# Performance work log

Hardware: AMD Instinct MI355X
Metric: run time of the kernel (lower is better)

The kernel has to match this reference:

```python
import jax, jax.numpy as jnp
import numpy as np

T_STEPS = 16384  # sequence length T
N_DIM = 256      # input channels n
M_DIM = 512      # hidden/reservoir size m
K_MEM = 511      # memory rows K (addresses are 0..K, row 0 = 'no memory op')
L_OUT = 256      # output dims L


def setup_inputs() -> dict:
    key = jax.random.key(0)
    ks = jax.random.split(key, 10)
    s_ih = 1.0 / np.sqrt(N_DIM)
    s_hh = 1.0 / np.sqrt(M_DIM)
    X = jax.random.normal(ks[0], (T_STEPS, N_DIM), jnp.float32)
    h0 = jnp.zeros((M_DIM,), jnp.float32)  # init_state = zeros(m)
    # torch.nn.GRU parameters (single layer): weight_ih [3m, n], weight_hh [3m, m]
    W_ih = jax.random.normal(ks[1], (3 * M_DIM, N_DIM), jnp.float32) * s_ih
    W_hh = jax.random.normal(ks[2], (3 * M_DIM, M_DIM), jnp.float32) * s_hh
    b_ih = jax.random.normal(ks[3], (3 * M_DIM,), jnp.float32) * s_hh
    b_hh = jax.random.normal(ks[4], (3 * M_DIM,), jnp.float32) * s_hh
    # C_: Linear(m, K+1) -> memory address logits
    C_w = jax.random.normal(ks[5], (K_MEM + 1, M_DIM), jnp.float32) * s_hh
    C_b = jax.random.normal(ks[6], (K_MEM + 1,), jnp.float32) * s_hh
    # V_: Linear(m, L) -> outputs
    V_w = jax.random.normal(ks[7], (L_OUT, M_DIM), jnp.float32) * s_hh
    V_b = jax.random.normal(ks[8], (L_OUT,), jnp.float32) * s_hh
    return {"X": X, "h0": h0, "W_ih": W_ih, "W_hh": W_hh, "b_ih": b_ih,
            "b_hh": b_hh, "C_w": C_w, "C_b": C_b, "V_w": V_w, "V_b": V_b}


def reference(X, h0, W_ih, W_hh, b_ih, b_hh, C_w, C_b, V_w, V_b):
    m = h0.shape[0]
    n_addr = C_b.shape[0]  # K + 1

    def step(carry, x):
        h, M, written = carry
        # GRU cell (torch semantics)
        gi = W_ih @ x + b_ih          # [3m]
        gh = W_hh @ h + b_hh          # [3m]
        i_r, i_z, i_n = jnp.split(gi, 3)
        h_r, h_z, h_n = jnp.split(gh, 3)
        r = jax.nn.sigmoid(i_r + h_r)
        z = jax.nn.sigmoid(i_z + h_z)
        ng = jnp.tanh(i_n + r * h_n)
        h_new = (1.0 - z) * ng + z * h
        # discrete memory addressing via argmax over C_(h)
        logits = C_w @ h_new + C_b    # [K+1]
        q = jnp.argmax(logits)
        mem_q = M[q]                  # gather (read before write)
        has_entry = written[q] & (q > 0)
        # if address already written: read memory, replacing h
        h_out = jnp.where(has_entry, mem_q, h_new)
        # if address new (and > 0): write h into memory
        do_write = (q > 0) & jnp.logical_not(written[q])
        write_val = jnp.where(do_write, h_new, mem_q)  # no-op write otherwise
        M = M.at[q].set(write_val)
        written = written.at[q].set(written[q] | (q > 0))
        return (h_out, M, written), h_out

    M0 = jnp.zeros((n_addr, m), X.dtype)       # q_0 = 0 -> memory starts empty
    written0 = jnp.zeros((n_addr,), jnp.bool_)
    _, H = jax.lax.scan(step, (h0, M0, written0), X)  # H: [T, m]
    Y = H @ V_w.T + V_b                          # [T, L]
    return Y
```

## Files before the change

### kernel.cpp

```cpp
#include <hip/hip_runtime.h>
#include <stdint.h>

#define T_STEPS 16384
#define NDIM 256
#define MDIM 512
#define KP1 512
#define LOUT 256
#define G 16
#define TPB 256

typedef unsigned long long u64;
typedef unsigned int u32;

constexpr size_t OFF_GH    = 0;
constexpr size_t OFF_GHS   = 512ull * 1536;
constexpr size_t OFF_M     = OFF_GHS + 1536;
constexpr size_t OFF_RING  = OFF_M + 512ull * 512;
constexpr size_t OFF_H     = OFF_RING + 4ull * 1536;
constexpr size_t OFF_VWT   = OFF_H + 16384ull * 512;
constexpr size_t OFF_FLAGS = OFF_VWT + 512ull * 256;

__device__ __forceinline__ float ld_cohf(const float* p) {
  return __hip_atomic_load(p, __ATOMIC_RELAXED, __HIP_MEMORY_SCOPE_AGENT);
}
__device__ __forceinline__ void st_cohf(float* p, float v) {
  __hip_atomic_store(p, v, __ATOMIC_RELAXED, __HIP_MEMORY_SCOPE_AGENT);
}
__device__ __forceinline__ u64 ld_flag(const u64* p) {
  return __hip_atomic_load(p, __ATOMIC_RELAXED, __HIP_MEMORY_SCOPE_AGENT);
}
__device__ __forceinline__ void st_flag_rel(u64* p, u64 v) {
  __hip_atomic_store(p, v, __ATOMIC_RELEASE, __HIP_MEMORY_SCOPE_AGENT);
}
__device__ __forceinline__ void st_flag_rlx(u64* p, u64 v) {
  __hip_atomic_store(p, v, __ATOMIC_RELAXED, __HIP_MEMORY_SCOPE_AGENT);
}

__device__ __forceinline__ float sigm(float x) {
  return __builtin_amdgcn_rcpf(1.0f + __expf(-x));
}
__device__ __forceinline__ float tanh_(float x) {
  return 1.0f - 2.0f * __builtin_amdgcn_rcpf(__expf(2.0f * x) + 1.0f);
}

template<int CTRL>
__device__ __forceinline__ u32 dppmax(u32 v) {
  u32 t = (u32)__builtin_amdgcn_update_dpp(0, (int)v, CTRL, 0xf, 0xf, true);
  return v > t ? v : t;
}
__device__ __forceinline__ u32 wave_max_u32(u32 v) {
  v = dppmax<0x111>(v);
  v = dppmax<0x112>(v);
  v = dppmax<0x114>(v);
  v = dppmax<0x118>(v);
  v = dppmax<0x142>(v);
  v = dppmax<0x143>(v);
  return (u32)__builtin_amdgcn_readlane((int)v, 63);
}
__device__ __forceinline__ u32 row16_max_u32(u32 v) {
  v = dppmax<0x111>(v);
  v = dppmax<0x112>(v);
  v = dppmax<0x114>(v);
  v = dppmax<0x118>(v);
  return (u32)__builtin_amdgcn_readlane((int)v, 15);
}

__global__ __launch_bounds__(TPB, 1) void dmm_main(
    const float* __restrict__ X, const float* __restrict__ h0,
    const float* __restrict__ W_ih, const float* __restrict__ W_hh,
    const float* __restrict__ b_ih, const float* __restrict__ b_hh,
    const float* __restrict__ C_w, const float* __restrict__ C_b,
    float* __restrict__ ws)
{
  const int b   = blockIdx.x;
  const int tid = threadIdx.x;
  const int w   = tid >> 6;
  const int l   = tid & 63;

  float* GH   = ws + OFF_GH;
  float* GHS  = ws + OFF_GHS;
  float* Mrow = ws + OFF_M;
  float* RING = ws + OFF_RING;
  float* H    = ws + OFF_H;
  u64*   F    = (u64*)(ws + OFF_FLAGS);

  __shared__ __align__(16) float hnew[MDIM];
  __shared__ __align__(16) float red[96 * 36];
  __shared__ u32 written[KP1];
  __shared__ u32 bcw;

  const int pw   = (w >= 1) ? (w - 1) : 0;
  const int rloc = pw * 32 + (l >> 4) * 8;
  float wih[8][16];
  {
    int rbase = 96 * b + rloc;
    int cbase = 16 * (l & 15);
#pragma unroll
    for (int i = 0; i < 8; i++)
#pragma unroll
      for (int k = 0; k < 16; k++)
        wih[i][k] = W_ih[(size_t)(rbase + i) * NDIM + cbase + k];
  }
  float bihr[8];
#pragma unroll
  for (int i = 0; i < 8; i++) bihr[i] = b_ih[96 * b + rloc + i];

  float cw[4][16];
  {
    int rbase = 32 * b + w * 8 + (l >> 5) * 4;
    int cbase = 16 * (l & 31);
#pragma unroll
    for (int i = 0; i < 4; i++)
#pragma unroll
      for (int k = 0; k < 16; k++)
        cw[i][k] = C_w[(size_t)(rbase + i) * MDIM + cbase + k];
  }

  for (int i = tid; i < KP1; i += TPB) written[i] = 0u;
  if (tid == 0) bcw = 0u;
  hnew[tid]       = h0[tid];
  hnew[tid + 256] = h0[tid + 256];
  __syncthreads();

  float xreg[16];
  auto prefetchX = [&](int s) {
    int cbase = 16 * (l & 15);
#pragma unroll
    for (int k = 0; k < 16; k++) xreg[k] = X[(size_t)s * NDIM + cbase + k];
  };

  auto produce_gi = [&](int s) {
    float p[8];
#pragma unroll
    for (int i = 0; i < 8; i++) {
      float a = 0.f;
#pragma unroll
      for (int k = 0; k < 16; k++) a = fmaf(wih[i][k], xreg[k], a);
      p[i] = a;
    }
#pragma unroll
    for (int off = 1; off <= 8; off <<= 1) {
#pragma unroll
      for (int i = 0; i < 8; i++) p[i] += __shfl_xor(p[i], off, 64);
    }
    if ((l & 15) == 0) {
      float* dst = &RING[(size_t)(s & 3) * 1536 + 96 * b + rloc];
#pragma unroll
      for (int i = 0; i < 8; i++) st_cohf(&dst[i], p[i] + bihr[i]);
    }
  };

  auto compute_gh = [&](float* dst) {
    int cb = 16 * (l & 31);
    float hr[16];
#pragma unroll
    for (int k = 0; k < 16; k += 4) *(float4*)&hr[k] = *(const float4*)&hnew[cb + k];
    int rb = 96 * b + w * 24 + (l >> 5) * 12;
    float p[12];
#pragma unroll
    for (int i = 0; i < 12; i++) {
      float a = 0.f;
      const float* wr = &W_hh[(size_t)(rb + i) * MDIM + cb];
#pragma unroll
      for (int k = 0; k < 16; k++) a = fmaf(wr[k], hr[k], a);
      p[i] = a;
    }
    int rl = w * 24 + (l >> 5) * 12;
    int lc = l & 31;
#pragma unroll
    for (int i = 0; i < 12; i++) red[(rl + i) * 36 + lc] = p[i];
    __syncthreads();
    if (tid < 96) {
      float a = 0.f;
#pragma unroll
      for (int k = 0; k < 32; k += 4) {
        float4 v = *(const float4*)&red[tid * 36 + k];
        a += v.x + v.y + v.z + v.w;
      }
      a += b_hh[96 * b + tid];
      st_cohf(&dst[96 * b + tid], a);
    }
    __syncthreads();
  };

  if (w >= 1) {
    prefetchX(0); produce_gi(0);
    prefetchX(1); produce_gi(1);
    prefetchX(2); produce_gi(2);
    prefetchX(3);
  }
  __syncthreads();
  compute_gh(GHS);
  if (tid == 0) st_flag_rel(&F[b], 1ull);
  if (w == 0) {
    int guard = 0;
    bool done = false;
    while (!done) {
      u64 v = (l < G) ? ld_flag(&F[l]) : 1ull;
      done = (__ballot((int)(v == 1ull)) == ~0ull);
      if (++guard > (1 << 22)) break;
    }
  }
  __syncthreads();

  const float* ghsrc = GHS;
  bool prevReadHit = false;
  int  qprev = 0;

  for (int t = 0; t < T_STEPS; ++t) {
    float g0 = ld_cohf(&ghsrc[tid]);
    float g1 = ld_cohf(&ghsrc[tid + 256]);
    float g2 = ld_cohf(&ghsrc[512 + tid]);
    float g3 = ld_cohf(&ghsrc[512 + tid + 256]);
    float g4 = ld_cohf(&ghsrc[1024 + tid]);
    float g5 = ld_cohf(&ghsrc[1024 + tid + 256]);
    float m0 = 0.f, m1 = 0.f;
    if (prevReadHit) {
      m0 = ld_cohf(&Mrow[(size_t)qprev * 512 + tid]);
      m1 = ld_cohf(&Mrow[(size_t)qprev * 512 + tid + 256]);
    }
    const float* gi = &RING[(size_t)(t & 3) * 1536];
    float i0 = ld_cohf(&gi[tid]);
    float i1 = ld_cohf(&gi[tid + 256]);
    float i2 = ld_cohf(&gi[512 + tid]);
    float i3 = ld_cohf(&gi[512 + tid + 256]);
    float i4 = ld_cohf(&gi[1024 + tid]);
    float i5 = ld_cohf(&gi[1024 + tid + 256]);

    if (prevReadHit && b == 0) {
      __builtin_nontemporal_store(m0, &H[(size_t)(t - 1) * 512 + tid]);
      __builtin_nontemporal_store(m1, &H[(size_t)(t - 1) * 512 + tid + 256]);
    }

    float hp0 = prevReadHit ? m0 : hnew[tid];
    float hp1 = prevReadHit ? m1 : hnew[tid + 256];
    float r0 = sigm(i0 + g0), r1 = sigm(i1 + g1);
    float z0 = sigm(i2 + g2), z1 = sigm(i3 + g3);
    float n0 = tanh_(fmaf(r0, g4, i4)), n1 = tanh_(fmaf(r1, g5, i5));
    float hn0 = fmaf(z0, hp0 - n0, n0);
    float hn1 = fmaf(z1, hp1 - n1, n1);
    hnew[tid]       = hn0;
    hnew[tid + 256] = hn1;
    __syncthreads();

    {
      int cb = 16 * (l & 31);
      float hr[16];
#pragma unroll
      for (int k = 0; k < 16; k += 4) *(float4*)&hr[k] = *(const float4*)&hnew[cb + k];
      float p0 = 0.f, p1 = 0.f, p2 = 0.f, p3 = 0.f;
#pragma unroll
      for (int k = 0; k < 16; k++) {
        p0 = fmaf(cw[0][k], hr[k], p0);
        p1 = fmaf(cw[1][k], hr[k], p1);
        p2 = fmaf(cw[2][k], hr[k], p2);
        p3 = fmaf(cw[3][k], hr[k], p3);
      }
      int rl = w * 8 + (l >> 5) * 4;
      int lc = l & 31;
      red[(rl + 0) * 36 + lc] = p0;
      red[(rl + 1) * 36 + lc] = p1;
      red[(rl + 2) * 36 + lc] = p2;
      red[(rl + 3) * 36 + lc] = p3;
    }
    __syncthreads();

    u64 ownkey = 0;
    if (w <= 1) {
      u32 ord = 0;
      if (l < 32) {
        const float4* rp = (const float4*)&red[l * 36];
        float4 v0 = rp[0], v1 = rp[1], v2 = rp[2], v3 = rp[3];
        float4 v4 = rp[4], v5 = rp[5], v6 = rp[6], v7 = rp[7];
        double d0 = ((double)v0.x + (double)v0.y) + ((double)v0.z + (double)v0.w);
        double d1 = ((double)v1.x + (double)v1.y) + ((double)v1.z + (double)v1.w);
        double d2 = ((double)v2.x + (double)v2.y) + ((double)v2.z + (double)v2.w);
        double d3 = ((double)v3.x + (double)v3.y) + ((double)v3.z + (double)v3.w);
        double d4 = ((double)v4.x + (double)v4.y) + ((double)v4.z + (double)v4.w);
        double d5 = ((double)v5.x + (double)v5.y) + ((double)v5.z + (double)v5.w);
        double d6 = ((double)v6.x + (double)v6.y) + ((double)v6.z + (double)v6.w);
        double d7 = ((double)v7.x + (double)v7.y) + ((double)v7.z + (double)v7.w);
        double a = (((d0 + d1) + (d2 + d3)) + ((d4 + d5) + (d6 + d7)))
                 + (double)C_b[32 * b + l];
        float af = (float)a;
        u32 bits = __float_as_uint(af);
        ord = (bits & 0x80000000u) ? ~bits : (bits | 0x80000000u);
      }
      u32 maxord = wave_max_u32(ord);
      u64 mask = __ballot((int)(ord == maxord));
      int lane = __builtin_ctzll(mask);
      u64 key41 = ((u64)maxord << 9) | (u64)(511 - (32 * b + lane));
      if (tid == 64)
        st_flag_rlx(&F[16 + (size_t)(t & 1) * 16 + b], ((u64)(t + 1) << 41) | key41);
      ownkey = key41;
    }

    if (w >= 1 && t + 3 < T_STEPS) {
      produce_gi(t + 3);
      if (t + 4 < T_STEPS) prefetchX(t + 4);
    }

    u32 info;
    if (w == 0) {
      const bool need = (l < G) && (l != b);
      const u64* fp = &F[16 + (size_t)(t & 1) * 16 + l];
      u64 vp = need ? ld_flag(fp) : 0;
      int guard = 0;
      u64 v;
      for (;;) {
        u64 vn = need ? ld_flag(fp) : 0;
        bool ok = !need || ((vp >> 41) == (u64)(t + 1));
        if (__ballot((int)ok) == ~0ull) { v = vp; break; }
        vp = vn;
        if (++guard > (1 << 22)) { v = vp; break; }
      }
      u64 key = (l < G) ? ((l == b) ? ownkey : (v & ((1ull << 41) - 1))) : 0;
      u32 o = (u32)(key >> 9);
      u32 maxo = row16_max_u32(o);
      u32 cand = (o == maxo && l < G) ? (u32)(key & 511u) : 0u;
      u32 best = row16_max_u32(cand);
      int q = 511 - (int)best;
      u32 vinfo = 0;
      if (l == 0) {
        u32 wr = written[q];
        u32 fresh = (q > 0 && wr == 0u) ? 1u : 0u;
        u32 rhit  = (q > 0 && wr != 0u) ? 1u : 0u;
        if (fresh) written[q] = 1u;
        vinfo = (u32)q | (fresh << 16) | (rhit << 17);
      }
      vinfo = (u32)__builtin_amdgcn_readfirstlane((int)vinfo);
      info = vinfo;
      if (l == 0)
        __hip_atomic_store(&bcw, (vinfo << 4) | ((u32)(t + 1) & 0xFu),
                           __ATOMIC_RELEASE, __HIP_MEMORY_SCOPE_WORKGROUP);
    } else {
      u32 v;
      int guard = 0;
      for (;;) {
        v = __hip_atomic_load(&bcw, __ATOMIC_ACQUIRE, __HIP_MEMORY_SCOPE_WORKGROUP);
        if ((v & 0xFu) == ((u32)(t + 1) & 0xFu)) break;
        if (++guard > (1 << 25)) break;
      }
      info = v >> 4;
    }
    int  q     = (int)(info & 0xFFFFu);
    bool fresh = (info >> 16) & 1u;
    bool rhit  = (info >> 17) & 1u;

    if (!rhit) {
      if (b == 0) {
        __builtin_nontemporal_store(hnew[tid], &H[(size_t)t * 512 + tid]);
        __builtin_nontemporal_store(hnew[tid + 256], &H[(size_t)t * 512 + tid + 256]);
      }
      float* dst;
      if (fresh) {
        if (tid < 32) st_cohf(&Mrow[(size_t)q * 512 + 32 * b + tid], hnew[32 * b + tid]);
        dst = &GH[(size_t)q * 1536];
      } else {
        dst = GHS;
      }
      compute_gh(dst);
      if (tid == 0) st_flag_rel(&F[48 + (size_t)(t & 1) * 16 + b], (u64)(t + 1));
      if (w == 0) {
        int guard = 0;
        for (;;) {
          u64 v = (l < G) ? ld_flag(&F[48 + (size_t)(t & 1) * 16 + l]) : 0;
          bool ok = (l >= G) || (v == (u64)(t + 1));
          if (__ballot((int)ok) == ~0ull) break;
          if (++guard > (1 << 22)) break;
        }
      }
      __syncthreads();
      ghsrc = dst;
      prevReadHit = false;
    } else {
      ghsrc = &GH[(size_t)q * 1536];
      prevReadHit = true;
      qprev = q;
    }
  }

  if (prevReadHit && b == 0) {
    float a = ld_cohf(&Mrow[(size_t)qprev * 512 + tid]);
    float c = ld_cohf(&Mrow[(size_t)qprev * 512 + tid + 256]);
    __builtin_nontemporal_store(a, &H[(size_t)(T_STEPS - 1) * 512 + tid]);
    __builtin_nontemporal_store(c, &H[(size_t)(T_STEPS - 1) * 512 + tid + 256]);
  }
}

__global__ void vw_transpose(const float* __restrict__ Vw, float* __restrict__ VwT) {
  int idx = blockIdx.x * 256 + threadIdx.x;
  int kk = idx >> 8, ll = idx & 255;
  VwT[idx] = Vw[(size_t)ll * MDIM + kk];
}

__global__ __launch_bounds__(256) void y_gemm(const float* __restrict__ Hm,
                                              const float* __restrict__ VwT,
                                              const float* __restrict__ Vb,
                                              float* __restrict__ Y) {
  int t0 = blockIdx.x * 16;
  int tid = threadIdx.x;
  __shared__ __align__(16) float hs[16 * MDIM];
  for (int i = tid; i < 16 * MDIM; i += 256)
    hs[i] = Hm[(size_t)t0 * MDIM + i];
  __syncthreads();
  float acc[16];
  float vb = Vb[tid];
#pragma unroll
  for (int r = 0; r < 16; r++) acc[r] = vb;
  for (int k = 0; k < MDIM; k += 4) {
    float v0 = VwT[(size_t)(k + 0) * LOUT + tid];
    float v1 = VwT[(size_t)(k + 1) * LOUT + tid];
    float v2 = VwT[(size_t)(k + 2) * LOUT + tid];
    float v3 = VwT[(size_t)(k + 3) * LOUT + tid];
#pragma unroll
    for (int r = 0; r < 16; r++) {
      float4 h4 = *(const float4*)&hs[r * MDIM + k];
      acc[r] = fmaf(h4.x, v0, fmaf(h4.y, v1, fmaf(h4.z, v2, fmaf(h4.w, v3, acc[r]))));
    }
  }
#pragma unroll
  for (int r = 0; r < 16; r++)
    Y[(size_t)(t0 + r) * LOUT + tid] = acc[r];
}

extern "C" void kernel_launch(void* const* d_in, const int* in_sizes, int n_in,
                              void* d_out, int out_size, void* d_ws, size_t ws_size,
                              hipStream_t stream) {
  const float* X    = (const float*)d_in[0];
  const float* h0   = (const float*)d_in[1];
  const float* W_ih = (const float*)d_in[2];
  const float* W_hh = (const float*)d_in[3];
  const float* b_ih = (const float*)d_in[4];
  const float* b_hh = (const float*)d_in[5];
  const float* C_w  = (const float*)d_in[6];
  const float* C_b  = (const float*)d_in[7];
  const float* V_w  = (const float*)d_in[8];
  const float* V_b  = (const float*)d_in[9];
  float* ws  = (float*)d_ws;
  float* VwT = ws + OFF_VWT;
  float* Hm  = ws + OFF_H;

  hipLaunchKernelGGL(vw_transpose, dim3(512), dim3(256), 0, stream, V_w, VwT);
  hipLaunchKernelGGL(dmm_main, dim3(G), dim3(TPB), 0, stream,
                     X, h0, W_ih, W_hh, b_ih, b_hh, C_w, C_b, ws);
  hipLaunchKernelGGL(y_gemm, dim3(T_STEPS / 16), dim3(256), 0, stream,
                     Hm, VwT, V_b, (float*)d_out);
}
```

Baseline: 43.15 ms.

## Pin recurrent blocks to one XCC and use sc0 flag loads/stores

Launches 256 blocks and lets the first 16 that land on XCC 0 claim worker slots through an atomic counter, so all cooperating blocks share one L2. It then tests whether flags written and read with sc0 (bypassing only the CU-local cache) propagate correctly. If they do, the per-step inter-block flag exchange uses these lighter loads and stores instead of agent-scope atomics, aiming to cut synchronization latency on the serial recurrence. It adds startup handshake overhead, relies on the hardware register for XCC id, and falls back to mixed-XCC placement with a timeout if too few blocks land on XCC 0.

```diff
diff --git a/kernel.cpp b/kernel.cpp
--- a/kernel.cpp
+++ b/kernel.cpp
@@ -8,6 +8,7 @@
 #define LOUT 256
 #define G 16
 #define TPB 256
+#define NBLK 256
 
 typedef unsigned long long u64;
 typedef unsigned int u32;
@@ -34,6 +35,25 @@
 }
 __device__ __forceinline__ void st_flag_rlx(u64* p, u64 v) {
   __hip_atomic_store(p, v, __ATOMIC_RELAXED, __HIP_MEMORY_SCOPE_AGENT);
+}
+
+__device__ __forceinline__ u64 ld64_sc0(const u64* p) {
+  u64 v;
+  asm volatile("global_load_dwordx2 %0, %1, off sc0\n\t"
+               "s_waitcnt vmcnt(0)"
+               : "=&v"(v) : "v"(p) : "memory");
+  return v;
+}
+__device__ __forceinline__ void st64_sc0(u64* p, u64 v) {
+  asm volatile("global_store_dwordx2 %0, %1, off sc0" :: "v"(p), "v"(v) : "memory");
+}
+__device__ __forceinline__ void drain_vm() {
+  asm volatile("s_waitcnt vmcnt(0)" ::: "memory");
+}
+
+#define HWREG_XCC_ID ((31u << 11) | 20u)
+__device__ __forceinline__ u32 xcc_id() {
+  return (u32)__builtin_amdgcn_s_getreg(HWREG_XCC_ID) & 0xFu;
 }
 
 __device__ __forceinline__ float sigm(float x) {
@@ -72,7 +92,6 @@
     const float* __restrict__ C_w, const float* __restrict__ C_b,
     float* __restrict__ ws)
 {
-  const int b   = blockIdx.x;
   const int tid = threadIdx.x;
   const int w   = tid >> 6;
   const int l   = tid & 63;
@@ -84,10 +103,84 @@
   float* H    = ws + OFF_H;
   u64*   F    = (u64*)(ws + OFF_FLAGS);
 
+  u32* Ecnt = (u32*)Mrow;
+  u64* Tst  = (u64*)(Mrow + 16);
+  u64* Md   = (u64*)(Mrow + 64);
+
   __shared__ __align__(16) float hnew[MDIM];
   __shared__ __align__(16) float red[96 * 36];
   __shared__ u32 written[KP1];
   __shared__ u32 bcw;
+  __shared__ int s_i;
+
+  if (tid == 0) {
+    u32 xcc = xcc_id();
+    int widx = -1;
+    if (xcc == 0) {
+      u32 r = __hip_atomic_fetch_add(Ecnt, 1u, __ATOMIC_RELAXED,
+                                     __HIP_MEMORY_SCOPE_AGENT);
+      if (r < (u32)G) widx = (int)r;
+    } else if (blockIdx.x < G) {
+      int guard = 0; u32 c;
+      do {
+        c = __hip_atomic_load(Ecnt, __ATOMIC_RELAXED, __HIP_MEMORY_SCOPE_AGENT);
+      } while (c < (u32)G && ++guard < (1 << 12));
+      if (c < (u32)G) {
+        u32 r = __hip_atomic_fetch_add(Ecnt, 1u, __ATOMIC_RELAXED,
+                                       __HIP_MEMORY_SCOPE_AGENT);
+        if (r < (u32)G) widx = (int)r;
+      }
+    }
+    s_i = widx;
+  }
+  __syncthreads();
+  const int b = s_i;
+  __syncthreads();
+  if (b < 0) return;
+
+  __shared__ int s_good;
+  if (tid == 0) s_good = 1;
+  __syncthreads();
+  for (int r = 1; r <= 8; ++r) {
+    if (tid == 0 && s_good) {
+      drain_vm();
+      st64_sc0(&Tst[b], (u64)r);
+    }
+    if (w == 0 && s_good) {
+      int guard = 0;
+      for (;;) {
+        u64 v = (u64)r;
+        if (l < G) v = ld64_sc0(&Tst[l]);
+        bool ok = (l >= G) || (v >= (u64)r);
+        if (__ballot((int)ok) == ~0ull) break;
+        if (++guard > (1 << 12)) { if (l == 0) s_good = 0; break; }
+      }
+    }
+    __syncthreads();
+  }
+  if (tid == 0)
+    __hip_atomic_store(&Md[b], 2ull | (u64)s_good, __ATOMIC_RELEASE,
+                       __HIP_MEMORY_SCOPE_AGENT);
+  if (w == 0) {
+    int guard = 0, moderes = 0;
+    for (;;) {
+      u64 v = 3ull;
+      if (l < G) v = __hip_atomic_load(&Md[l], __ATOMIC_ACQUIRE,
+                                       __HIP_MEMORY_SCOPE_AGENT);
+      bool ok = (l >= G) || ((v & 2ull) != 0);
+      if (__ballot((int)ok) == ~0ull) {
+        u64 bm = __ballot((int)((v & 1ull) != 0));
+        moderes = (bm == ~0ull) ? 1 : 0;
+        break;
+      }
+      if (++guard > (1 << 20)) { moderes = 0; break; }
+    }
+    if (l == 0) s_i = moderes;
+  }
+  __syncthreads();
+  const bool SC0F = (s_i != 0);
+  const int GSTEP = SC0F ? (1 << 12) : (1 << 22);
+
 
   const int pw   = (w >= 1) ? (w - 1) : 0;
   const int rloc = pw * 32 + (l >> 4) * 8;
@@ -194,10 +287,9 @@
   if (tid == 0) st_flag_rel(&F[b], 1ull);
   if (w == 0) {
     int guard = 0;
-    bool done = false;
-    while (!done) {
+    for (;;) {
       u64 v = (l < G) ? ld_flag(&F[l]) : 1ull;
-      done = (__ballot((int)(v == 1ull)) == ~0ull);
+      if (__ballot((int)(v == 1ull)) == ~0ull) break;
       if (++guard > (1 << 22)) break;
     }
   }
@@ -290,8 +382,11 @@
       u64 mask = __ballot((int)(ord == maxord));
       int lane = __builtin_ctzll(mask);
       u64 key41 = ((u64)maxord << 9) | (u64)(511 - (32 * b + lane));
-      if (tid == 64)
-        st_flag_rlx(&F[16 + (size_t)(t & 1) * 16 + b], ((u64)(t + 1) << 41) | key41);
+      if (tid == 64) {
+        u64 fv = ((u64)(t + 1) << 41) | key41;
+        u64* fp = &F[16 + (size_t)(t & 1) * 16 + b];
+        if (SC0F) st64_sc0(fp, fv); else st_flag_rlx(fp, fv);
+      }
       ownkey = key41;
     }
 
@@ -304,15 +399,25 @@
     if (w == 0) {
       const bool need = (l < G) && (l != b);
       const u64* fp = &F[16 + (size_t)(t & 1) * 16 + l];
-      u64 vp = need ? ld_flag(fp) : 0;
-      int guard = 0;
-      u64 v;
-      for (;;) {
-        u64 vn = need ? ld_flag(fp) : 0;
-        bool ok = !need || ((vp >> 41) == (u64)(t + 1));
-        if (__ballot((int)ok) == ~0ull) { v = vp; break; }
-        vp = vn;
-        if (++guard > (1 << 22)) { v = vp; break; }
+      u64 v = 0;
+      if (SC0F) {
+        int guard = 0;
+        for (;;) {
+          if (need) v = ld64_sc0(fp);
+          bool ok = !need || ((v >> 41) == (u64)(t + 1));
+          if (__ballot((int)ok) == ~0ull) break;
+          if (++guard > GSTEP) break;
+        }
+      } else {
+        u64 vp = need ? ld_flag(fp) : 0;
+        int guard = 0;
+        for (;;) {
+          u64 vn = need ? ld_flag(fp) : 0;
+          bool ok = !need || ((vp >> 41) == (u64)(t + 1));
+          if (__ballot((int)ok) == ~0ull) { v = vp; break; }
+          vp = vn;
+          if (++guard > GSTEP) { v = vp; break; }
+        }
       }
       u64 key = (l < G) ? ((l == b) ? ownkey : (v & ((1ull << 41) - 1))) : 0;
       u32 o = (u32)(key >> 9);
@@ -360,14 +465,21 @@
         dst = GHS;
       }
       compute_gh(dst);
-      if (tid == 0) st_flag_rel(&F[48 + (size_t)(t & 1) * 16 + b], (u64)(t + 1));
+      if (tid == 0) {
+        u64* fp = &F[48 + (size_t)(t & 1) * 16 + b];
+        if (SC0F) { drain_vm(); st64_sc0(fp, (u64)(t + 1)); }
+        else st_flag_rel(fp, (u64)(t + 1));
+      }
       if (w == 0) {
         int guard = 0;
         for (;;) {
-          u64 v = (l < G) ? ld_flag(&F[48 + (size_t)(t & 1) * 16 + l]) : 0;
+          u64 v;
+          const u64* fp = &F[48 + (size_t)(t & 1) * 16 + l];
+          if (l < G) v = SC0F ? ld64_sc0(fp) : ld_flag(fp);
+          else v = (u64)(t + 1);
           bool ok = (l >= G) || (v == (u64)(t + 1));
           if (__ballot((int)ok) == ~0ull) break;
-          if (++guard > (1 << 22)) break;
+          if (++guard > GSTEP) break;
         }
       }
       __syncthreads();
@@ -390,6 +502,10 @@
 
 __global__ void vw_transpose(const float* __restrict__ Vw, float* __restrict__ VwT) {
   int idx = blockIdx.x * 256 + threadIdx.x;
+  if (blockIdx.x == 0) {
+    float* M0 = VwT - (OFF_VWT - OFF_M);
+    M0[threadIdx.x] = 0.f;
+  }
   int kk = idx >> 8, ll = idx & 255;
   VwT[idx] = Vw[(size_t)ll * MDIM + kk];
 }
@@ -442,7 +558,7 @@
   float* Hm  = ws + OFF_H;
 
   hipLaunchKernelGGL(vw_transpose, dim3(512), dim3(256), 0, stream, V_w, VwT);
-  hipLaunchKernelGGL(dmm_main, dim3(G), dim3(TPB), 0, stream,
+  hipLaunchKernelGGL(dmm_main, dim3(NBLK), dim3(TPB), 0, stream,
                      X, h0, W_ih, W_hh, b_ih, b_hh, C_w, C_b, ws);
   hipLaunchKernelGGL(y_gemm, dim3(T_STEPS / 16), dim3(256), 0, stream,
                      Hm, VwT, V_b, (float*)d_out);
```

After: 40.87 ms. 1.06x faster.
